# Kernel optimization log

Measured on AMD Instinct MI355X. Metric: run time of the kernel, lower is better.

Reference implementation:

```python
import jax, jax.numpy as jnp
import numpy as np
from jax.scipy.linalg import expm

D_DYN = 512
STATIC_DIM = 64
U_DIM = 32
N_OBS = 20 * 2 + 10  # num_prod*2 + num_inj
BATCH = 512
T_STEPS = 256


def setup_inputs() -> dict:
    key = jax.random.key(0)
    ks = jax.random.split(key, 9)
    d = D_DYN
    return {
        "z_dyn": jax.random.normal(ks[0], (BATCH, d), jnp.float32),
        "z_static": jax.random.normal(ks[1], (BATCH, STATIC_DIM), jnp.float32),
        "dt": jax.random.uniform(ks[2], (1, 1), jnp.float32),
        "U": jax.random.normal(ks[3], (T_STEPS, BATCH, U_DIM), jnp.float32),
        "A_skew_params": (jax.random.normal(ks[4], (d * (d - 1) // 2,), jnp.float32) * 0.01),
        "gamma_raw": jnp.ones((d,), jnp.float32) * 0.5,
        "B_ct": jax.random.normal(ks[5], (d, U_DIM), jnp.float32) * (1.0 / np.sqrt(U_DIM)),
        "C": jax.random.normal(ks[6], (N_OBS, d), jnp.float32) * (1.0 / np.sqrt(d)),
        "D": jax.random.normal(ks[7], (N_OBS, U_DIM), jnp.float32) * (1.0 / np.sqrt(U_DIM)),
    }


def reference(z_dyn, z_static, dt, U, A_skew_params, gamma_raw, B_ct, C, D):
    d = z_dyn.shape[1]
    # Build continuous-time generator: skew-symmetric part minus positive diagonal damping.
    iu = jnp.triu_indices(d, k=1)
    A_skew = jnp.zeros((d, d), A_skew_params.dtype).at[iu].set(A_skew_params)
    A_skew = A_skew - A_skew.T
    A_ct = A_skew - jnp.diag(jax.nn.softplus(gamma_raw))
    # Exact ZOH discretization: A_bar = expm(A*dt), B_bar = A^{-1}(A_bar - I) B
    dt_val = dt[0, 0]
    A_bar = expm(A_ct * dt_val)
    B_bar = jnp.linalg.solve(A_ct, (A_bar - jnp.eye(d, dtype=A_ct.dtype)) @ B_ct)
    A_bar_T, B_bar_T, C_T, D_T = A_bar.T, B_bar.T, C.T, D.T

    def step(z, ut):
        z = z @ A_bar_T + ut @ B_bar_T          # [B, d]
        y = z @ C_T + (ut * dt) @ D_T           # [B, n_obs]
        return z, (z, y)

    _, (Z, Y) = jax.lax.scan(step, z_dyn, U)    # Z: [T, B, d], Y: [T, B, n_obs]
    return Z, Y
```

## Files before the change

### kernel.cpp

```cpp
#include <hip/hip_runtime.h>
#include <stdint.h>


typedef __bf16 bf16x8 __attribute__((ext_vector_type(8)));
typedef float  f32x4  __attribute__((ext_vector_type(4)));

#define NE  576
#define NE3 1728

__device__ __forceinline__ unsigned short f2bf(float x){
  union { float f; unsigned int u; } v; v.f = x;
  unsigned int r = (v.u + 0x7fffu + ((v.u >> 16) & 1u)) >> 16;
  return (unsigned short)r;
}
__device__ __forceinline__ float bf2f(unsigned short h){
  union { float f; unsigned int u; } v; v.u = ((unsigned int)h) << 16;
  return v.f;
}

__device__ __forceinline__ void gll16(const void* g, void* l){
  __builtin_amdgcn_global_load_lds((__attribute__((address_space(1))) void*)g,
                                   (__attribute__((address_space(3))) void*)l,
                                   16, 0, 0);
}

__global__ __launch_bounds__(256) void k_build_M(
    const float* __restrict__ skew, const float* __restrict__ gamma,
    const float* __restrict__ dtp, const float* __restrict__ B_ct,
    float* __restrict__ Xf, unsigned short* __restrict__ XAp,
    unsigned short* __restrict__ XBt){
  __shared__ float T[32][33];
  int bx = blockIdx.x % 18, by = blockIdx.x / 18;
  int r0 = by * 32, c0 = bx * 32;
  int tr = threadIdx.x >> 5, tc = threadIdx.x & 31;
  float sc = dtp[0] * 0.25f;
  #pragma unroll
  for (int p = 0; p < 4; p++) {
    int r = r0 + p * 8 + tr, c = c0 + tc;
    float v = 0.f;
    if (r < 512 && c < 512) {
      if (r < c) {
        long k = 511L * r - (long)r * (r - 1) / 2 + (c - r - 1);
        v = skew[k];
      } else if (r > c) {
        long k = 511L * c - (long)c * (c - 1) / 2 + (r - c - 1);
        v = -skew[k];
      } else {
        float g = gamma[r];
        float sp = (g > 20.f) ? g : log1pf(expf(g));
        v = -sp;
      }
    } else if (r < 512 && c >= 512 && c < 544) {
      v = B_ct[r * 32 + (c - 512)];
    }
    v *= sc;
    long id = (long)r * NE + c;
    Xf[id] = v;
    unsigned short hi = f2bf(v);
    unsigned short lo = f2bf(v - bf2f(hi));
    XAp[(long)r * NE3 + c]          = hi;
    XAp[(long)r * NE3 + NE + c]     = hi;
    XAp[(long)r * NE3 + 2 * NE + c] = lo;
    T[p * 8 + tr][tc] = v;
  }
  __syncthreads();
  #pragma unroll
  for (int p = 0; p < 4; p++) {
    int cl = p * 8 + tr, rl = tc;
    float v = T[rl][cl];
    unsigned short hi = f2bf(v);
    unsigned short lo = f2bf(v - bf2f(hi));
    long base = (long)(c0 + cl) * NE3 + r0;
    XBt[base + rl]          = hi;
    XBt[base + NE + rl]     = lo;
    XBt[base + 2 * NE + rl] = hi;
  }
}

__global__ __launch_bounds__(256) void k_expm_gemm(
    const unsigned short* __restrict__ Ap, const unsigned short* __restrict__ Bt,
    const float* __restrict__ Cadd, float* __restrict__ outF,
    unsigned short* __restrict__ outAp, unsigned short* __restrict__ outBt){
  __shared__ __align__(16) unsigned short As[2][32 * 192];
  __shared__ __align__(16) unsigned short Bs[2][32 * 192];
  int tid = threadIdx.x, wave = tid >> 6, lane = tid & 63;
  int wm = wave & 1, wn = wave >> 1;
  int m0 = blockIdx.y * 32, n0 = blockIdx.x * 32;
  int lr = lane & 15, kq = lane >> 4;
  f32x4 acc = {0.f, 0.f, 0.f, 0.f};
  auto stage = [&](int buf, int kt){
    #pragma unroll
    for (int i = 0; i < 3; i++) {
      int base = i * 256 + wave * 64;
      int cc = base + lane;
      int rr = cc / 24, sl = cc - rr * 24;
      int ss = (sl & 24) | ((sl & 7) ^ (rr & 7));
      gll16(Ap + (long)(m0 + rr) * NE3 + kt + ss * 8, &As[buf][base * 8]);
      gll16(Bt + (long)(n0 + rr) * NE3 + kt + ss * 8, &Bs[buf][base * 8]);
    }
  };
  stage(0, 0);
  int cur = 0;
  for (int kt = 0; kt < NE3; kt += 192) {
    if (kt + 192 < NE3) {
      stage(cur ^ 1, kt + 192);
      asm volatile("s_waitcnt vmcnt(6)" ::: "memory");
    } else {
      asm volatile("s_waitcnt vmcnt(0)" ::: "memory");
    }
    __builtin_amdgcn_s_barrier();
    __builtin_amdgcn_sched_barrier(0);
    #pragma unroll
    for (int hh = 0; hh < 6; hh++) {
      int eo = (hh * 32 + kq * 8) ^ ((lr & 7) << 3);
      bf16x8 af = *(const bf16x8*)&As[cur][(wm * 16 + lr) * 192 + eo];
      bf16x8 bf = *(const bf16x8*)&Bs[cur][(wn * 16 + lr) * 192 + eo];
      acc = __builtin_amdgcn_mfma_f32_16x16x32_bf16(af, bf, acc, 0, 0, 0);
    }
    __builtin_amdgcn_s_barrier();
    cur ^= 1;
  }
  int n = n0 + wn * 16 + lr;
  for (int i = 0; i < 4; i++) {
    int m = m0 + wm * 16 + kq * 4 + i;
    float v = acc[i];
    if (Cadd) v += Cadd[(long)m * NE + n];
    if (outF) outF[(long)m * NE + n] = v;
    unsigned short hi = f2bf(v);
    unsigned short lo = f2bf(v - bf2f(hi));
    if (outAp) {
      outAp[(long)m * NE3 + n]          = hi;
      outAp[(long)m * NE3 + NE + n]     = hi;
      outAp[(long)m * NE3 + 2 * NE + n] = lo;
    }
    if (outBt) {
      outBt[(long)n * NE3 + m]          = hi;
      outBt[(long)n * NE3 + NE + m]     = lo;
      outBt[(long)n * NE3 + 2 * NE + m] = hi;
    }
  }
}

__global__ __launch_bounds__(256) void k_poly(
    const float* __restrict__ Xf, const float* __restrict__ X2f,
    const float* __restrict__ X3f, float* __restrict__ B0,
    unsigned short* __restrict__ B1Ap){
  int id = blockIdx.x * 256 + threadIdx.x;
  if (id >= NE * NE) return;
  int r = id / NE, c = id % NE;
  float x = Xf[id], x2 = X2f[id], x3 = X3f[id];
  float ii = (r == c) ? 1.f : 0.f;
  float b0 = ii + x + x2 * 0.5f + x3 * (1.f / 6.f);
  float b1 = ii * (1.f / 24.f) + x * (1.f / 120.f) + x2 * (1.f / 720.f) + x3 * (1.f / 5040.f);
  B0[id] = b0;
  unsigned short hi = f2bf(b1), lo = f2bf(b1 - bf2f(hi));
  B1Ap[(long)r * NE3 + c]          = hi;
  B1Ap[(long)r * NE3 + NE + c]     = hi;
  B1Ap[(long)r * NE3 + 2 * NE + c] = lo;
}

__global__ __launch_bounds__(256) void k_extract(
    const float* __restrict__ F, const float* __restrict__ Cin,
    unsigned short* __restrict__ WbigT, unsigned short* __restrict__ PT1,
    unsigned short* __restrict__ BbarT, unsigned short* __restrict__ G0,
    unsigned short* __restrict__ CA0){
  int b = blockIdx.x;
  if (b < 256) {
    __shared__ float T[32][33];
    int by = b >> 4, bx = b & 15;
    int m0 = by * 32, k0 = bx * 32;
    int tr = threadIdx.x >> 5, tc = threadIdx.x & 31;
    #pragma unroll
    for (int p = 0; p < 4; p++) {
      int m = m0 + p * 8 + tr, k = k0 + tc;
      float v = F[(long)m * NE + k];
      WbigT[(long)m * 1024 + k] = f2bf(v);
      T[p * 8 + tr][tc] = v;
    }
    __syncthreads();
    #pragma unroll
    for (int p = 0; p < 4; p++) {
      int kl = p * 8 + tr, ml = tc;
      PT1[(long)(k0 + kl) * 512 + m0 + ml] = f2bf(T[ml][kl]);
    }
  } else {
    int id0 = (b - 256) * 256 + threadIdx.x;
    for (int id = id0; id < 64 * 512; id += 1024) {
      if (id < 512 * 32) {
        int dd = id >> 5, u = id & 31;
        unsigned short h = f2bf(F[(long)dd * NE + 512 + u]);
        G0[id] = h;
        BbarT[(long)u * 512 + dd] = h;
      }
      CA0[id] = (id < 50 * 512) ? f2bf(Cin[id]) : (unsigned short)0;
    }
  }
}

template<int BM, int BN, int WM, int WN>
__global__ __launch_bounds__(256) void k_btgemm(
    const unsigned short* __restrict__ A, int ldA, long sAz,
    const unsigned short* __restrict__ Bt, int ldB, long sBz,
    unsigned short* __restrict__ C, int ldC, long sCz, int K,
    unsigned short* __restrict__ outT, int ldT, long sTz){
  constexpr int FM = BM / (16 * WM), FN = BN / (16 * WN);
  constexpr int LA = BM / 32, LB = BN / 32;
  __shared__ __align__(16) unsigned short As[2][BM * 64];
  __shared__ __align__(16) unsigned short Bs[2][BN * 64];
  int tid = threadIdx.x, wave = tid >> 6, lane = tid & 63;
  int wm = wave % WM, wn = wave / WM;
  long z = blockIdx.z;
  const unsigned short* Ab = A + z * sAz;
  const unsigned short* Bb = Bt + z * sBz;
  int m0 = blockIdx.y * BM, n0 = blockIdx.x * BN;
  int lr = lane & 15, kq = lane >> 4;
  f32x4 acc[FM][FN];
  f32x4 z4 = {0.f, 0.f, 0.f, 0.f};
  for (int i = 0; i < FM; i++) for (int j = 0; j < FN; j++) acc[i][j] = z4;
  auto stage = [&](int buf, int kt){
    #pragma unroll
    for (int i = 0; i < LA; i++) {
      int base = i * 256 + wave * 64;
      int cc = base + lane; int rr = cc >> 3, sl = cc & 7;
      gll16(Ab + (long)(m0 + rr) * ldA + kt + ((sl ^ (rr & 7)) << 3), &As[buf][base * 8]);
    }
    #pragma unroll
    for (int i = 0; i < LB; i++) {
      int base = i * 256 + wave * 64;
      int cc = base + lane; int rr = cc >> 3, sl = cc & 7;
      gll16(Bb + (long)(n0 + rr) * ldB + kt + ((sl ^ (rr & 7)) << 3), &Bs[buf][base * 8]);
    }
  };
  stage(0, 0);
  int cur = 0;
  for (int kt = 0; kt < K; kt += 64) {
    if (kt + 64 < K) {
      stage(cur ^ 1, kt + 64);
      asm volatile("s_waitcnt vmcnt(%0)" :: "i"(LA + LB) : "memory");
    } else {
      asm volatile("s_waitcnt vmcnt(0)" ::: "memory");
    }
    __builtin_amdgcn_s_barrier();
    __builtin_amdgcn_sched_barrier(0);
    #pragma unroll
    for (int h = 0; h < 2; h++) {
      int eo = (h * 32 + kq * 8) ^ ((lr & 7) << 3);
      bf16x8 af[FM], bfr[FN];
      #pragma unroll
      for (int i = 0; i < FM; i++)
        af[i] = *(const bf16x8*)&As[cur][(wm * (16 * FM) + i * 16 + lr) * 64 + eo];
      #pragma unroll
      for (int j = 0; j < FN; j++)
        bfr[j] = *(const bf16x8*)&Bs[cur][(wn * (16 * FN) + j * 16 + lr) * 64 + eo];
      #pragma unroll
      for (int i = 0; i < FM; i++)
        #pragma unroll
        for (int j = 0; j < FN; j++)
          acc[i][j] = __builtin_amdgcn_mfma_f32_16x16x32_bf16(af[i], bfr[j], acc[i][j], 0, 0, 0);
    }
    __builtin_amdgcn_s_barrier();
    cur ^= 1;
  }
  unsigned short* Cb = C + z * sCz;
  unsigned short* Tb = outT ? outT + z * sTz : nullptr;
  for (int i = 0; i < FM; i++)
    for (int j = 0; j < FN; j++) {
      int n = n0 + wn * (16 * FN) + j * 16 + lr;
      for (int r = 0; r < 4; r++) {
        int m = m0 + wm * (16 * FM) + i * 16 + kq * 4 + r;
        unsigned short hv = f2bf(acc[i][j][r]);
        Cb[(long)m * ldC + n] = hv;
        if (Tb) Tb[(long)n * ldT + m] = hv;
      }
    }
}

__global__ __launch_bounds__(256) void k_assembleUW(
    const unsigned short* __restrict__ G, const unsigned short* __restrict__ CA,
    const unsigned short* __restrict__ CG, const float* __restrict__ Din,
    const float* __restrict__ dtp, unsigned short* __restrict__ WbigT){
  long e = ((long)blockIdx.x * 256 + threadIdx.x) << 2;
  if (e < 4194304) {
    int n = (int)(e >> 9), kk2 = (int)(e & 511);
    int j = (n >> 9) + 1, dcol = n & 511;
    int i = (kk2 >> 5) + 1, uu = kk2 & 31;
    ushort4 h = {0, 0, 0, 0};
    if (i <= j) h = *(const ushort4*)&G[(long)(j - i) * 16384 + dcol * 32 + uu];
    *(ushort4*)&WbigT[(long)n * 1024 + 512 + kk2] = h;
  } else {
    int id2 = (int)(e - 4194304);
    int np = id2 >> 10, kp = id2 & 1023;
    int jm1 = np >> 6, o = np & 63;
    ushort4 h;
    if (kp < 512) {
      h = *(const ushort4*)&CA[(long)(jm1 + 1) * 32768 + o * 512 + kp];
    } else {
      int i = ((kp - 512) >> 5) + 1, u = kp & 31;
      float f0 = 0.f, f1 = 0.f, f2 = 0.f, f3 = 0.f;
      if (i <= jm1 + 1) {
        ushort4 g = *(const ushort4*)&CG[(long)(jm1 + 1 - i) * 2048 + o * 32 + u];
        f0 = bf2f(g.x); f1 = bf2f(g.y); f2 = bf2f(g.z); f3 = bf2f(g.w);
      }
      if (i == jm1 + 1 && o < 50) {
        float s = dtp[0];
        f0 += s * Din[o * 32 + u];     f1 += s * Din[o * 32 + u + 1];
        f2 += s * Din[o * 32 + u + 2]; f3 += s * Din[o * 32 + u + 3];
      }
      h.x = f2bf(f0); h.y = f2bf(f1); h.z = f2bf(f2); h.w = f2bf(f3);
    }
    *(ushort4*)&WbigT[(long)(8192 + np) * 1024 + kp] = h;
  }
}

__global__ __launch_bounds__(256) void k_packX(
    const float* __restrict__ zdyn, const float* __restrict__ U,
    unsigned short* __restrict__ Xbuf){
  long id4 = (long)blockIdx.x * 256 + threadIdx.x;
  if (id4 < 1048576) {
    long e = id4 << 2;
    long c = e >> 18; int rem = (int)(e & 262143);
    int bb = rem >> 9, kk2 = rem & 511;
    int t = (int)(c * 16) + (kk2 >> 5), uu = kk2 & 31;
    float4 v = *(const float4*)&U[((long)t * 512 + bb) * 32 + uu];
    ushort4 h; h.x = f2bf(v.x); h.y = f2bf(v.y); h.z = f2bf(v.z); h.w = f2bf(v.w);
    *(ushort4*)&Xbuf[c * 524288 + (long)bb * 1024 + 512 + kk2] = h;
  } else {
    long e = (id4 - 1048576) << 2;
    if (e < 262144) {
      int bb = (int)(e >> 9), col = (int)(e & 511);
      float4 v = *(const float4*)&zdyn[(long)bb * 512 + col];
      ushort4 h; h.x = f2bf(v.x); h.y = f2bf(v.y); h.z = f2bf(v.z); h.w = f2bf(v.w);
      *(ushort4*)&Xbuf[(long)bb * 1024 + col] = h;
    }
  }
}

__global__ __launch_bounds__(256) void k_scanround(
    const unsigned short* __restrict__ Sin, int ldS, long sS,
    const unsigned short* __restrict__ R, int ldR,
    unsigned short* __restrict__ Out, int ldO, long sO, int h){
  __shared__ __align__(16) unsigned short As[2][64 * 64];
  __shared__ __align__(16) unsigned short Bs[2][64 * 64];
  int tid = threadIdx.x, wave = tid >> 6, lane = tid & 63;
  int wm = wave & 1, wn = wave >> 1;
  int c = blockIdx.z;
  int m0 = blockIdx.y * 64, n0 = blockIdx.x * 64;
  int lr = lane & 15, kq = lane >> 4;
  f32x4 acc[2][2];
  f32x4 z4 = {0.f, 0.f, 0.f, 0.f};
  for (int i = 0; i < 2; i++) for (int j = 0; j < 2; j++) acc[i][j] = z4;
  if (c >= h) {
    const unsigned short* Ab = Sin + (long)(c - h) * sS;
    auto stage = [&](int buf, int kt){
      #pragma unroll
      for (int i = 0; i < 2; i++) {
        int base = i * 256 + wave * 64;
        int cc = base + lane; int rr = cc >> 3, sl = cc & 7;
        gll16(Ab + (long)(m0 + rr) * ldS + kt + ((sl ^ (rr & 7)) << 3), &As[buf][base * 8]);
      }
      #pragma unroll
      for (int i = 0; i < 2; i++) {
        int base = i * 256 + wave * 64;
        int cc = base + lane; int rr = cc >> 3, sl = cc & 7;
        gll16(R + (long)(n0 + rr) * ldR + kt + ((sl ^ (rr & 7)) << 3), &Bs[buf][base * 8]);
      }
    };
    stage(0, 0);
    int cur = 0;
    for (int kt = 0; kt < 512; kt += 64) {
      if (kt + 64 < 512) {
        stage(cur ^ 1, kt + 64);
        asm volatile("s_waitcnt vmcnt(4)" ::: "memory");
      } else {
        asm volatile("s_waitcnt vmcnt(0)" ::: "memory");
      }
      __builtin_amdgcn_s_barrier();
      __builtin_amdgcn_sched_barrier(0);
      #pragma unroll
      for (int h2 = 0; h2 < 2; h2++) {
        int eo = (h2 * 32 + kq * 8) ^ ((lr & 7) << 3);
        bf16x8 af[2], bfr[2];
        #pragma unroll
        for (int i = 0; i < 2; i++)
          af[i] = *(const bf16x8*)&As[cur][(wm * 32 + i * 16 + lr) * 64 + eo];
        #pragma unroll
        for (int j = 0; j < 2; j++)
          bfr[j] = *(const bf16x8*)&Bs[cur][(wn * 32 + j * 16 + lr) * 64 + eo];
        #pragma unroll
        for (int i = 0; i < 2; i++)
          #pragma unroll
          for (int j = 0; j < 2; j++)
            acc[i][j] = __builtin_amdgcn_mfma_f32_16x16x32_bf16(af[i], bfr[j], acc[i][j], 0, 0, 0);
      }
      __builtin_amdgcn_s_barrier();
      cur ^= 1;
    }
  }
  const unsigned short* inC = Sin + (long)c * sS;
  unsigned short* OB = Out + (long)c * sO;
  for (int j = 0; j < 2; j++) {
    int n = n0 + wn * 32 + j * 16 + lr;
    for (int i = 0; i < 2; i++)
      for (int r = 0; r < 4; r++) {
        int m = m0 + wm * 32 + i * 16 + kq * 4 + r;
        float v = acc[i][j][r] + bf2f(inC[(long)m * ldS + n]);
        OB[(long)m * ldO + n] = f2bf(v);
      }
  }
}

__global__ __launch_bounds__(512, 4) void k_mmbig(
    const unsigned short* __restrict__ Xall, const unsigned short* __restrict__ W,
    float* __restrict__ Zout, float* __restrict__ Yout){
  __shared__ __align__(16) unsigned short As[2][128 * 64];
  __shared__ __align__(16) unsigned short Bs[2][128 * 64];
  int tid = threadIdx.x, wave = tid >> 6, lane = tid & 63;
  int wm = wave & 1, wn = wave >> 1;
  int c = blockIdx.z;
  const unsigned short* Xc = Xall + (long)c * 524288;
  int m0 = blockIdx.y * 128, n0 = blockIdx.x * 128;
  int lr = lane & 15, kq = lane >> 4;
  f32x4 acc[4][2];
  f32x4 z4 = {0.f, 0.f, 0.f, 0.f};
  for (int i = 0; i < 4; i++) for (int j = 0; j < 2; j++) acc[i][j] = z4;
  auto stage = [&](int buf, int kt){
    #pragma unroll
    for (int i = 0; i < 2; i++) {
      int cc = i * 512 + tid;
      int rr = cc >> 3, sl = cc & 7;
      gll16(Xc + (long)(m0 + rr) * 1024 + kt + ((sl ^ (rr & 7)) << 3), &As[buf][cc * 8]);
    }
    #pragma unroll
    for (int i = 0; i < 2; i++) {
      int cc = i * 512 + tid;
      int rr = cc >> 3, sl = cc & 7;
      gll16(W + (long)(n0 + rr) * 1024 + kt + ((sl ^ (rr & 7)) << 3), &Bs[buf][cc * 8]);
    }
  };
  stage(0, 0);
  int cur = 0;
  for (int kt = 0; kt < 1024; kt += 64) {
    if (kt + 64 < 1024) {
      stage(cur ^ 1, kt + 64);
      asm volatile("s_waitcnt vmcnt(4)" ::: "memory");
    } else {
      asm volatile("s_waitcnt vmcnt(0)" ::: "memory");
    }
    __builtin_amdgcn_s_barrier();
    __builtin_amdgcn_sched_barrier(0);
    #pragma unroll
    for (int h = 0; h < 2; h++) {
      int eo = (h * 32 + kq * 8) ^ ((lr & 7) << 3);
      bf16x8 af[4], bfr[2];
      #pragma unroll
      for (int i = 0; i < 4; i++)
        af[i] = *(const bf16x8*)&As[cur][(wm * 64 + i * 16 + lr) * 64 + eo];
      #pragma unroll
      for (int j = 0; j < 2; j++)
        bfr[j] = *(const bf16x8*)&Bs[cur][(wn * 32 + j * 16 + lr) * 64 + eo];
      #pragma unroll
      for (int i = 0; i < 4; i++)
        #pragma unroll
        for (int j = 0; j < 2; j++)
          acc[i][j] = __builtin_amdgcn_mfma_f32_16x16x32_bf16(af[i], bfr[j], acc[i][j], 0, 0, 0);
    }
    __builtin_amdgcn_s_barrier();
    cur ^= 1;
  }
  int t0 = c * 16;
  if (n0 < 8192) {
    int jm1 = n0 >> 9;
    float* Zt = Zout + (long)(t0 + jm1) * 262144;
    for (int j = 0; j < 2; j++) {
      int n = n0 + wn * 32 + j * 16 + lr, dcol = n & 511;
      for (int i = 0; i < 4; i++)
        for (int r = 0; r < 4; r++) {
          int m = m0 + wm * 64 + i * 16 + kq * 4 + r;
          Zt[(long)m * 512 + dcol] = acc[i][j][r];
        }
    }
  } else {
    for (int j = 0; j < 2; j++) {
      int n = n0 + wn * 32 + j * 16 + lr;
      int q = n - 8192, jm1 = q >> 6, o = q & 63;
      if (o >= 50) continue;
      int t = t0 + jm1;
      for (int i = 0; i < 4; i++)
        for (int r = 0; r < 4; r++) {
          int m = m0 + wm * 64 + i * 16 + kq * 4 + r;
          Yout[((long)t * 512 + m) * 50 + o] = acc[i][j][r];
        }
    }
  }
}

static constexpr long NE2F = 331776L * 4;
static constexpr long SPLT = 995328L * 2;
static constexpr long OFF_XF   = 0;
static constexpr long OFF_X2F  = OFF_XF   + NE2F;
static constexpr long OFF_X3F  = OFF_X2F  + NE2F;
static constexpr long OFF_B0F  = OFF_X3F  + NE2F;
static constexpr long OFF_XAP  = OFF_B0F  + NE2F;
static constexpr long OFF_XBT  = OFF_XAP  + SPLT;
static constexpr long OFF_X2AP = OFF_XBT  + SPLT;
static constexpr long OFF_X2BT = OFF_X2AP + SPLT;
static constexpr long OFF_X4BT = OFF_X2BT + SPLT;
static constexpr long OFF_B1AP = OFF_X4BT + SPLT;
static constexpr long OFF_EAP  = OFF_B1AP + SPLT;
static constexpr long OFF_EBT  = OFF_EAP  + SPLT;
static constexpr long OFF_FAP  = OFF_EBT  + SPLT;
static constexpr long OFF_FBT  = OFF_FAP  + SPLT;
static constexpr long OFF_FF   = OFF_FBT  + SPLT;
static constexpr long OFF_WBT  = 0;
static constexpr long OFF_PT   = 18874368;
static constexpr long OFF_BBT  = OFF_PT  + 16L * 262144 * 2;
static constexpr long OFF_G    = OFF_BBT + 32768;
static constexpr long OFF_CA   = OFF_G   + 16L * 16384 * 2;
static constexpr long OFF_CG   = OFF_CA  + 17L * 32768 * 2;
static constexpr long OFF_XB   = OFF_PT;

extern "C" void kernel_launch(void* const* d_in, const int* in_sizes, int n_in,
                              void* d_out, int out_size, void* d_ws, size_t ws_size,
                              hipStream_t stream){
  const float* z_dyn = (const float*)d_in[0];
  const float* dtp   = (const float*)d_in[2];
  const float* U     = (const float*)d_in[3];
  const float* skew  = (const float*)d_in[4];
  const float* gamma = (const float*)d_in[5];
  const float* B_ct  = (const float*)d_in[6];
  const float* Cin   = (const float*)d_in[7];
  const float* Din   = (const float*)d_in[8];
  float* Zout = (float*)d_out;
  float* Yout = Zout + 67108864L;

  char* ws = (char*)d_ws;
  float* Xf  = (float*)(ws + OFF_XF);
  float* X2f = (float*)(ws + OFF_X2F);
  float* X3f = (float*)(ws + OFF_X3F);
  float* B0f = (float*)(ws + OFF_B0F);
  float* Ff  = (float*)(ws + OFF_FF);
  unsigned short* XAp  = (unsigned short*)(ws + OFF_XAP);
  unsigned short* XBt  = (unsigned short*)(ws + OFF_XBT);
  unsigned short* X2Ap = (unsigned short*)(ws + OFF_X2AP);
  unsigned short* X2Bt = (unsigned short*)(ws + OFF_X2BT);
  unsigned short* X4Bt = (unsigned short*)(ws + OFF_X4BT);
  unsigned short* B1Ap = (unsigned short*)(ws + OFF_B1AP);
  unsigned short* EAp  = (unsigned short*)(ws + OFF_EAP);
  unsigned short* EBt  = (unsigned short*)(ws + OFF_EBT);
  unsigned short* FAp  = (unsigned short*)(ws + OFF_FAP);
  unsigned short* FBt  = (unsigned short*)(ws + OFF_FBT);
  unsigned short* WbigT = (unsigned short*)(ws + OFF_WBT);
  unsigned short* PT    = (unsigned short*)(ws + OFF_PT);
  unsigned short* BbarT = (unsigned short*)(ws + OFF_BBT);
  unsigned short* Gar   = (unsigned short*)(ws + OFF_G);
  unsigned short* CAb   = (unsigned short*)(ws + OFF_CA);
  unsigned short* CGb   = (unsigned short*)(ws + OFF_CG);
  unsigned short* Xb    = (unsigned short*)(ws + OFF_XB);

  unsigned short* Sb  = (unsigned short*)Yout;
  unsigned short* M2b = Sb  + 4194304;
  unsigned short* TM2 = M2b + 262144;
  unsigned short* M4b = TM2 + 262144;
  unsigned short* TM4 = M4b + 262144;
  unsigned short* M8b = TM4 + 262144;

  dim3 b256(256);
  dim3 gE(18, 18);
  const long WBLK = 524288;
  const long PBLK = 262144;
  unsigned short* Wlast = WbigT + 15L * WBLK;

  k_build_M<<<dim3(324), b256, 0, stream>>>(skew, gamma, dtp, B_ct, Xf, XAp, XBt);
  k_expm_gemm<<<gE, b256, 0, stream>>>(XAp,  XBt,  nullptr, X2f, X2Ap, X2Bt);
  k_expm_gemm<<<gE, b256, 0, stream>>>(X2Ap, XBt,  nullptr, X3f, nullptr, nullptr);
  k_expm_gemm<<<gE, b256, 0, stream>>>(X2Ap, X2Bt, nullptr, nullptr, nullptr, X4Bt);
  k_poly<<<dim3(1296), b256, 0, stream>>>(Xf, X2f, X3f, B0f, B1Ap);
  k_expm_gemm<<<gE, b256, 0, stream>>>(B1Ap, X4Bt, B0f, nullptr, EAp, EBt);
  k_expm_gemm<<<gE, b256, 0, stream>>>(EAp, EBt, nullptr, nullptr, FAp, FBt);
  k_expm_gemm<<<gE, b256, 0, stream>>>(FAp, FBt, nullptr, Ff, nullptr, nullptr);

  k_extract<<<dim3(260), b256, 0, stream>>>(Ff, Cin, WbigT, PT, BbarT, Gar, CAb);

  k_btgemm<64,64,2,2><<<dim3(8,8,1), b256, 0, stream>>>(WbigT, 1024, 0, PT, 512, 0, WbigT + WBLK, 1024, 0, 512, PT + PBLK, 512, 0);
  k_btgemm<64,64,2,2><<<dim3(8,8,2), b256, 0, stream>>>(WbigT + WBLK, 1024, 0, PT, 512, PBLK, WbigT + 2*WBLK, 1024, WBLK, 512, PT + 2*PBLK, 512, PBLK);
  k_btgemm<64,64,2,2><<<dim3(8,8,4), b256, 0, stream>>>(WbigT + 3*WBLK, 1024, 0, PT, 512, PBLK, WbigT + 4*WBLK, 1024, WBLK, 512, PT + 4*PBLK, 512, PBLK);
  k_btgemm<64,64,2,2><<<dim3(8,8,8), b256, 0, stream>>>(WbigT + 7*WBLK, 1024, 0, PT, 512, PBLK, WbigT + 8*WBLK, 1024, WBLK, 512, PT + 8*PBLK, 512, PBLK);

  k_btgemm<64,64,2,2><<<dim3(8,8,1), b256, 0, stream>>>(Wlast, 1024, 0, PT + 15*PBLK, 512, 0, M2b, 512, 0, 512, TM2, 512, 0);
  k_btgemm<64,64,2,2><<<dim3(8,8,1), b256, 0, stream>>>(M2b, 512, 0, TM2, 512, 0, M4b, 512, 0, 512, TM4, 512, 0);
  k_btgemm<64,64,2,2><<<dim3(8,8,1), b256, 0, stream>>>(M4b, 512, 0, TM4, 512, 0, M8b, 512, 0, 512, nullptr, 0, 0);

  k_btgemm<64,32,4,1><<<dim3(1,8,15), b256, 0, stream>>>(WbigT, 1024, WBLK, BbarT, 512, 0, Gar + 16384, 32, 16384, 512, nullptr, 0, 0);
  k_btgemm<64,64,2,2><<<dim3(8,1,8), b256, 0, stream>>>(CAb, 512, 0, PT, 512, PBLK, CAb + 32768, 512, 32768, 512, nullptr, 0, 0);
  k_btgemm<64,64,2,2><<<dim3(8,1,8), b256, 0, stream>>>(CAb + 32768, 512, 32768, PT + 7*PBLK, 512, 0, CAb + 9L*32768, 512, 32768, 512, nullptr, 0, 0);
  k_btgemm<64,32,4,1><<<dim3(1,1,16), b256, 0, stream>>>(CAb, 512, 32768, BbarT, 512, 0, CGb, 32, 2048, 512, nullptr, 0, 0);

  k_assembleUW<<<dim3(5120), b256, 0, stream>>>(Gar, CAb, CGb, Din, dtp, WbigT);
  k_packX<<<dim3(4353), b256, 0, stream>>>(z_dyn, U, Xb);

  k_btgemm<64,64,2,2><<<dim3(8,8,15), b256, 0, stream>>>(
      Xb + 512, 1024, WBLK, Wlast + 512, 1024, 0,
      Xb + WBLK, 1024, WBLK, 512, nullptr, 0, 0);

  k_scanround<<<dim3(8,8,16), b256, 0, stream>>>(Xb, 1024, WBLK, Wlast, 1024, Sb, 512, PBLK, 1);
  k_scanround<<<dim3(8,8,16), b256, 0, stream>>>(Sb, 512, PBLK, M2b, 512, Xb, 1024, WBLK, 2);
  k_scanround<<<dim3(8,8,16), b256, 0, stream>>>(Xb, 1024, WBLK, M4b, 512, Sb, 512, PBLK, 4);
  k_scanround<<<dim3(8,8,16), b256, 0, stream>>>(Sb, 512, PBLK, M8b, 512, Xb, 1024, WBLK, 8);

  k_mmbig<<<dim3(72, 4, 16), dim3(512), 0, stream>>>(Xb, WbigT, Zout, Yout);
}
```

Before: 695.9 us.

## Skip zero K-blocks in big GEMM and merge small launches

The final big GEMM now bounds its K loop per output column block, so it skips the zero upper-triangular blocks of the Toeplitz-structured weight matrix. Independent expm GEMMs are batched into one launch through blockIdx.z. The G and CA GEMMs are merged into a new kernel, and the CG GEMM is fused with the input packing kernel. Together these are meant to remove wasted MFMA work and launch overhead. The risk is that an off-by-one in kmax, or a workspace overlap from the moved buffer offsets, corrupts results.

```diff
diff --git a/kernel.cpp b/kernel.cpp
--- a/kernel.cpp
+++ b/kernel.cpp
@@ -78,9 +78,18 @@
 }
 
 __global__ __launch_bounds__(256) void k_expm_gemm(
-    const unsigned short* __restrict__ Ap, const unsigned short* __restrict__ Bt,
-    const float* __restrict__ Cadd, float* __restrict__ outF,
-    unsigned short* __restrict__ outAp, unsigned short* __restrict__ outBt){
+    const unsigned short* __restrict__ Ap0, const unsigned short* __restrict__ Bt0,
+    const float* __restrict__ Cadd0, float* __restrict__ outF0,
+    unsigned short* __restrict__ outAp0, unsigned short* __restrict__ outBt0,
+    const unsigned short* __restrict__ Ap1, const unsigned short* __restrict__ Bt1,
+    const float* __restrict__ Cadd1, float* __restrict__ outF1,
+    unsigned short* __restrict__ outAp1, unsigned short* __restrict__ outBt1){
+  const unsigned short* Ap = Ap0;  const unsigned short* Bt = Bt0;
+  const float* Cadd = Cadd0;       float* outF = outF0;
+  unsigned short* outAp = outAp0;  unsigned short* outBt = outBt0;
+  if (blockIdx.z) {
+    Ap = Ap1; Bt = Bt1; Cadd = Cadd1; outF = outF1; outAp = outAp1; outBt = outBt1;
+  }
   __shared__ __align__(16) unsigned short As[2][32 * 192];
   __shared__ __align__(16) unsigned short Bs[2][32 * 192];
   int tid = threadIdx.x, wave = tid >> 6, lane = tid & 63;
@@ -273,6 +282,113 @@
         if (Tb) Tb[(long)n * ldT + m] = hv;
       }
     }
+}
+
+__device__ __forceinline__ void gemm6432(
+    const unsigned short* __restrict__ Ab, int ldA,
+    const unsigned short* __restrict__ Bb, int ldB,
+    unsigned short* __restrict__ Cb, int ldC, int m0, int n0,
+    unsigned short* As, unsigned short* Bs){
+  int tid = threadIdx.x, wave = tid >> 6, lane = tid & 63;
+  int wm = wave & 3;
+  int lr = lane & 15, kq = lane >> 4;
+  f32x4 acc[2];
+  f32x4 z4 = {0.f, 0.f, 0.f, 0.f};
+  acc[0] = z4; acc[1] = z4;
+  auto stage = [&](int buf, int kt){
+    #pragma unroll
+    for (int i = 0; i < 2; i++) {
+      int cc = i * 256 + tid; int rr = cc >> 3, sl = cc & 7;
+      gll16(Ab + (long)(m0 + rr) * ldA + kt + ((sl ^ (rr & 7)) << 3), As + buf * 4096 + cc * 8);
+    }
+    {
+      int cc = tid; int rr = cc >> 3, sl = cc & 7;
+      gll16(Bb + (long)(n0 + rr) * ldB + kt + ((sl ^ (rr & 7)) << 3), Bs + buf * 2048 + cc * 8);
+    }
+  };
+  stage(0, 0);
+  int cur = 0;
+  for (int kt = 0; kt < 512; kt += 64) {
+    if (kt + 64 < 512) {
+      stage(cur ^ 1, kt + 64);
+      asm volatile("s_waitcnt vmcnt(3)" ::: "memory");
+    } else {
+      asm volatile("s_waitcnt vmcnt(0)" ::: "memory");
+    }
+    __builtin_amdgcn_s_barrier();
+    __builtin_amdgcn_sched_barrier(0);
+    #pragma unroll
+    for (int h = 0; h < 2; h++) {
+      int eo = (h * 32 + kq * 8) ^ ((lr & 7) << 3);
+      bf16x8 af = *(const bf16x8*)&As[cur * 4096 + (wm * 16 + lr) * 64 + eo];
+      #pragma unroll
+      for (int j = 0; j < 2; j++) {
+        bf16x8 bfv = *(const bf16x8*)&Bs[cur * 2048 + (j * 16 + lr) * 64 + eo];
+        acc[j] = __builtin_amdgcn_mfma_f32_16x16x32_bf16(af, bfv, acc[j], 0, 0, 0);
+      }
+    }
+    __builtin_amdgcn_s_barrier();
+    cur ^= 1;
+  }
+  for (int j = 0; j < 2; j++) {
+    int n = n0 + j * 16 + lr;
+    for (int r = 0; r < 4; r++) {
+      int m = m0 + wm * 16 + kq * 4 + r;
+      Cb[(long)m * ldC + n] = f2bf(acc[j][r]);
+    }
+  }
+}
+
+__global__ __launch_bounds__(256) void k_gca(
+    const unsigned short* __restrict__ Wbig, const unsigned short* __restrict__ BbarT,
+    const unsigned short* __restrict__ CAb, const unsigned short* __restrict__ PT,
+    unsigned short* __restrict__ G1, unsigned short* __restrict__ CAout){
+  __shared__ __align__(16) unsigned short As[2 * 64 * 64];
+  __shared__ __align__(16) unsigned short Bs[2 * 32 * 64];
+  int z = blockIdx.z;
+  if (z < 15) {
+    if (blockIdx.x) return;
+    gemm6432(Wbig + (long)z * 524288, 1024, BbarT, 512,
+             G1 + (long)z * 16384, 32, blockIdx.y * 64, 0, As, Bs);
+  } else {
+    if (blockIdx.y) return;
+    int zz = z - 15;
+    gemm6432(CAb, 512, PT + (long)zz * 262144, 512,
+             CAout + (long)zz * 32768, 512, 0, blockIdx.x * 32, As, Bs);
+  }
+}
+
+__global__ __launch_bounds__(256) void k_cgpack(
+    const unsigned short* __restrict__ CAb, const unsigned short* __restrict__ BbarT,
+    unsigned short* __restrict__ CGb,
+    const float* __restrict__ zdyn, const float* __restrict__ Uin,
+    unsigned short* __restrict__ Xbuf){
+  int b = blockIdx.x;
+  if (b < 16) {
+    __shared__ __align__(16) unsigned short As[2 * 64 * 64];
+    __shared__ __align__(16) unsigned short Bs[2 * 32 * 64];
+    gemm6432(CAb + (long)b * 32768, 512, BbarT, 512,
+             CGb + (long)b * 2048, 32, 0, 0, As, Bs);
+    return;
+  }
+  long id4 = (long)(b - 16) * 256 + threadIdx.x;
+  if (id4 < 1048576) {
+    long e = id4 << 2;
+    long c = e >> 18; int rem = (int)(e & 262143);
+    int bb = rem >> 9, kk2 = rem & 511;
+    int t = (int)(c * 16) + (kk2 >> 5), uu = kk2 & 31;
+    float4 v = *(const float4*)&Uin[((long)t * 512 + bb) * 32 + uu];
+    ushort4 h; h.x = f2bf(v.x); h.y = f2bf(v.y); h.z = f2bf(v.z); h.w = f2bf(v.w);
+    *(ushort4*)&Xbuf[c * 524288 + (long)bb * 1024 + 512 + kk2] = h;
+  } else {
+    long e = (id4 - 1048576) << 2;
+    if (e < 262144) {
+      int bb = (int)(e >> 9), col = (int)(e & 511);
+      float4 v = *(const float4*)&zdyn[(long)bb * 512 + col];
+      ushort4 h; h.x = f2bf(v.x); h.y = f2bf(v.y); h.z = f2bf(v.z); h.w = f2bf(v.w);
+      *(ushort4*)&Xbuf[(long)bb * 1024 + col] = h;
+    }
+  }
 }
 
 __global__ __launch_bounds__(256) void k_assembleUW(
@@ -312,29 +428,6 @@
   }
 }
 
-__global__ __launch_bounds__(256) void k_packX(
-    const float* __restrict__ zdyn, const float* __restrict__ U,
-    unsigned short* __restrict__ Xbuf){
-  long id4 = (long)blockIdx.x * 256 + threadIdx.x;
-  if (id4 < 1048576) {
-    long e = id4 << 2;
-    long c = e >> 18; int rem = (int)(e & 262143);
-    int bb = rem >> 9, kk2 = rem & 511;
-    int t = (int)(c * 16) + (kk2 >> 5), uu = kk2 & 31;
-    float4 v = *(const float4*)&U[((long)t * 512 + bb) * 32 + uu];
-    ushort4 h; h.x = f2bf(v.x); h.y = f2bf(v.y); h.z = f2bf(v.z); h.w = f2bf(v.w);
-    *(ushort4*)&Xbuf[c * 524288 + (long)bb * 1024 + 512 + kk2] = h;
-  } else {
-    long e = (id4 - 1048576) << 2;
-    if (e < 262144) {
-      int bb = (int)(e >> 9), col = (int)(e & 511);
-      float4 v = *(const float4*)&zdyn[(long)bb * 512 + col];
-      ushort4 h; h.x = f2bf(v.x); h.y = f2bf(v.y); h.z = f2bf(v.z); h.w = f2bf(v.w);
-      *(ushort4*)&Xbuf[(long)bb * 1024 + col] = h;
-    }
-  }
-}
-
 __global__ __launch_bounds__(256) void k_scanround(
     const unsigned short* __restrict__ Sin, int ldS, long sS,
     const unsigned short* __restrict__ R, int ldR,
@@ -419,6 +512,13 @@
   int c = blockIdx.z;
   const unsigned short* Xc = Xall + (long)c * 524288;
   int m0 = blockIdx.y * 128, n0 = blockIdx.x * 128;
+  int kmax;
+  if (n0 < 8192) {
+    int j = (n0 >> 9) + 1;
+    kmax = (512 + 32 * j + 63) & ~63;
+  } else {
+    kmax = 576 + ((n0 - 8192) >> 1);
+  }
   int lr = lane & 15, kq = lane >> 4;
   f32x4 acc[4][2];
   f32x4 z4 = {0.f, 0.f, 0.f, 0.f};
@@ -439,8 +539,8 @@
   };
   stage(0, 0);
   int cur = 0;
-  for (int kt = 0; kt < 1024; kt += 64) {
-    if (kt + 64 < 1024) {
+  for (int kt = 0; kt < kmax; kt += 64) {
+    if (kt + 64 < kmax) {
       stage(cur ^ 1, kt + 64);
       asm volatile("s_waitcnt vmcnt(4)" ::: "memory");
     } else {
@@ -513,11 +613,11 @@
 static constexpr long OFF_FF   = OFF_FBT  + SPLT;
 static constexpr long OFF_WBT  = 0;
 static constexpr long OFF_PT   = 18874368;
-static constexpr long OFF_BBT  = OFF_PT  + 16L * 262144 * 2;
+static constexpr long OFF_XB   = OFF_PT;
+static constexpr long OFF_BBT  = 35651584;
 static constexpr long OFF_G    = OFF_BBT + 32768;
 static constexpr long OFF_CA   = OFF_G   + 16L * 16384 * 2;
 static constexpr long OFF_CG   = OFF_CA  + 17L * 32768 * 2;
-static constexpr long OFF_XB   = OFF_PT;
 
 extern "C" void kernel_launch(void* const* d_in, const int* in_sizes, int n_in,
                               void* d_out, int out_size, void* d_ws, size_t ws_size,
@@ -565,19 +665,23 @@
   unsigned short* M8b = TM4 + 262144;
 
   dim3 b256(256);
-  dim3 gE(18, 18);
   const long WBLK = 524288;
   const long PBLK = 262144;
   unsigned short* Wlast = WbigT + 15L * WBLK;
+  const unsigned short* NUL = nullptr;
 
   k_build_M<<<dim3(324), b256, 0, stream>>>(skew, gamma, dtp, B_ct, Xf, XAp, XBt);
-  k_expm_gemm<<<gE, b256, 0, stream>>>(XAp,  XBt,  nullptr, X2f, X2Ap, X2Bt);
-  k_expm_gemm<<<gE, b256, 0, stream>>>(X2Ap, XBt,  nullptr, X3f, nullptr, nullptr);
-  k_expm_gemm<<<gE, b256, 0, stream>>>(X2Ap, X2Bt, nullptr, nullptr, nullptr, X4Bt);
+  k_expm_gemm<<<dim3(18,18,1), b256, 0, stream>>>(XAp, XBt, nullptr, X2f, X2Ap, X2Bt,
+                                                  NUL, NUL, nullptr, nullptr, nullptr, nullptr);
+  k_expm_gemm<<<dim3(18,18,2), b256, 0, stream>>>(X2Ap, XBt,  nullptr, X3f, nullptr, nullptr,
+                                                  X2Ap, X2Bt, nullptr, nullptr, nullptr, X4Bt);
   k_poly<<<dim3(1296), b256, 0, stream>>>(Xf, X2f, X3f, B0f, B1Ap);
-  k_expm_gemm<<<gE, b256, 0, stream>>>(B1Ap, X4Bt, B0f, nullptr, EAp, EBt);
-  k_expm_gemm<<<gE, b256, 0, stream>>>(EAp, EBt, nullptr, nullptr, FAp, FBt);
-  k_expm_gemm<<<gE, b256, 0, stream>>>(FAp, FBt, nullptr, Ff, nullptr, nullptr);
+  k_expm_gemm<<<dim3(18,18,1), b256, 0, stream>>>(B1Ap, X4Bt, B0f, nullptr, EAp, EBt,
+                                                  NUL, NUL, nullptr, nullptr, nullptr, nullptr);
+  k_expm_gemm<<<dim3(18,18,1), b256, 0, stream>>>(EAp, EBt, nullptr, nullptr, FAp, FBt,
+                                                  NUL, NUL, nullptr, nullptr, nullptr, nullptr);
+  k_expm_gemm<<<dim3(18,18,1), b256, 0, stream>>>(FAp, FBt, nullptr, Ff, nullptr, nullptr,
+                                                  NUL, NUL, nullptr, nullptr, nullptr, nullptr);
 
   k_extract<<<dim3(260), b256, 0, stream>>>(Ff, Cin, WbigT, PT, BbarT, Gar, CAb);
 
@@ -590,13 +694,12 @@
   k_btgemm<64,64,2,2><<<dim3(8,8,1), b256, 0, stream>>>(M2b, 512, 0, TM2, 512, 0, M4b, 512, 0, 512, TM4, 512, 0);
   k_btgemm<64,64,2,2><<<dim3(8,8,1), b256, 0, stream>>>(M4b, 512, 0, TM4, 512, 0, M8b, 512, 0, 512, nullptr, 0, 0);
 
-  k_btgemm<64,32,4,1><<<dim3(1,8,15), b256, 0, stream>>>(WbigT, 1024, WBLK, BbarT, 512, 0, Gar + 16384, 32, 16384, 512, nullptr, 0, 0);
-  k_btgemm<64,64,2,2><<<dim3(8,1,8), b256, 0, stream>>>(CAb, 512, 0, PT, 512, PBLK, CAb + 32768, 512, 32768, 512, nullptr, 0, 0);
+  k_gca<<<dim3(16, 8, 23), b256, 0, stream>>>(WbigT, BbarT, CAb, PT, Gar + 16384, CAb + 32768);
   k_btgemm<64,64,2,2><<<dim3(8,1,8), b256, 0, stream>>>(CAb + 32768, 512, 32768, PT + 7*PBLK, 512, 0, CAb + 9L*32768, 512, 32768, 512, nullptr, 0, 0);
-  k_btgemm<64,32,4,1><<<dim3(1,1,16), b256, 0, stream>>>(CAb, 512, 32768, BbarT, 512, 0, CGb, 32, 2048, 512, nullptr, 0, 0);
+
+  k_cgpack<<<dim3(4368), b256, 0, stream>>>(CAb, BbarT, CGb, z_dyn, U, Xb);
 
   k_assembleUW<<<dim3(5120), b256, 0, stream>>>(Gar, CAb, CGb, Din, dtp, WbigT);
-  k_packX<<<dim3(4353), b256, 0, stream>>>(z_dyn, U, Xb);
 
   k_btgemm<64,64,2,2><<<dim3(8,8,15), b256, 0, stream>>>(
       Xb + 512, 1024, WBLK, Wlast + 512, 1024, 0,
```

After: 632.7 us. -9.1%, faster.
